# Kernel optimization log

Hardware: AMD Instinct MI355X
Metric: run time of the kernel (lower is better)

Reference implementation:

```python
import jax, jax.numpy as jnp
import numpy as np
from jax.ops import segment_sum

N_NODES = 50000
N_EDGES = 800000
D = 128
N_LAYERS = 3
N_GRAPHS = 256


def setup_inputs() -> dict:
    key = jax.random.key(0)
    k1, k2, k3, k4, k5, k6 = jax.random.split(key, 6)
    feats = jax.random.normal(k1, (N_NODES, D), dtype=jnp.float32)
    src = jax.random.randint(k2, (N_EDGES,), 0, N_NODES)
    dst = jax.random.randint(k3, (N_EDGES,), 0, N_NODES)
    graph_ids = jnp.sort(jax.random.randint(k4, (N_NODES,), 0, N_GRAPHS))
    W = jax.random.normal(k5, (N_LAYERS, D, D), dtype=jnp.float32) / np.float32(np.sqrt(D))
    b = jax.random.normal(k6, (N_LAYERS, D), dtype=jnp.float32) * 0.01
    return {"feats": feats, "W": W, "b": b, "src": src, "dst": dst, "graph_ids": graph_ids}


def reference(feats, W, b, src, dst, graph_ids):
    # DGL GraphConv with norm='both': h' = act(D_in^{-1/2} A D_out^{-1/2} h W + b)
    ones_e = jnp.ones((src.shape[0],), dtype=feats.dtype)
    deg_out = jnp.clip(segment_sum(ones_e, src, num_segments=N_NODES), 1.0)  # [N]
    deg_in = jnp.clip(segment_sum(ones_e, dst, num_segments=N_NODES), 1.0)   # [N]
    norm_out = jax.lax.rsqrt(deg_out)[:, None]  # [N,1]
    norm_in = jax.lax.rsqrt(deg_in)[:, None]    # [N,1]

    h = feats
    for l in range(N_LAYERS):
        hn = h * norm_out                                  # source-side norm
        agg = segment_sum(hn[src], dst, num_segments=N_NODES)  # SpMM gather/scatter
        agg = agg * norm_in                                # dest-side norm
        h = jax.nn.relu(agg @ W[l] + b[l])                 # [N,D]

    # AvgPooling readout: per-graph mean over nodes
    ones_n = jnp.ones((N_NODES,), dtype=h.dtype)
    counts = jnp.clip(segment_sum(ones_n, graph_ids, num_segments=N_GRAPHS), 1.0)
    pooled = segment_sum(h, graph_ids, num_segments=N_GRAPHS) / counts[:, None]
    return pooled  # [N_GRAPHS, D]
```

## Files before the change

### kernel.cpp

```cpp
#include <hip/hip_runtime.h>
#include <hip/hip_fp16.h>

#define DD 128
#define GG 256
#define RANGES 4
#define RSMAX 12544
#define NCHUNK 64

typedef _Float16 half8 __attribute__((ext_vector_type(8)));
typedef float floatx4 __attribute__((ext_vector_type(4)));

__device__ inline uint2 pack_half4(float4 v) {
    __half2 a = __floats2half2_rn(v.x, v.y);
    __half2 b = __floats2half2_rn(v.z, v.w);
    uint2 u;
    u.x = *reinterpret_cast<unsigned int*>(&a);
    u.y = *reinterpret_cast<unsigned int*>(&b);
    return u;
}

__global__ __launch_bounds__(256) void k_key(const int* __restrict__ src, const int* __restrict__ dst,
                                             unsigned int* __restrict__ key, int E) {
    int i = (blockIdx.x * 256 + threadIdx.x) * 4;
    if (i + 3 < E) {
        int4 s4 = *(const int4*)&src[i];
        int4 d4 = *(const int4*)&dst[i];
        uint4 k4;
        k4.x = (unsigned int)s4.x | ((unsigned int)d4.x << 16);
        k4.y = (unsigned int)s4.y | ((unsigned int)d4.y << 16);
        k4.z = (unsigned int)s4.z | ((unsigned int)d4.z << 16);
        k4.w = (unsigned int)s4.w | ((unsigned int)d4.w << 16);
        *(uint4*)&key[i] = k4;
    } else {
        for (int j = 0; j < 4 && i + j < E; ++j)
            key[i + j] = (unsigned int)src[i + j] | ((unsigned int)dst[i + j] << 16);
    }
}

__global__ __launch_bounds__(256) void k_hist2(const unsigned int* __restrict__ key,
                                               unsigned int* __restrict__ pk,
                                               int E, int N, int C, int RS, int L) {
    __shared__ unsigned int h[RSMAX];
    int r = blockIdx.x / C;
    int c = blockIdx.x % C;
    int r0 = r * RS;
    int r1 = min(r0 + RS, N);
    int nb = r1 - r0;
    for (int i = threadIdx.x; i < nb; i += 256) h[i] = 0;
    __syncthreads();
    int e0 = c * L, e1 = min(e0 + L, E);
    for (int e = e0 + threadIdx.x * 4; e < e1; e += 1024) {
        if (e + 3 < e1) {
            uint4 k4 = *(const uint4*)&key[e];
            #pragma unroll
            for (int j = 0; j < 4; ++j) {
                unsigned int kk = (j == 0) ? k4.x : (j == 1) ? k4.y : (j == 2) ? k4.z : k4.w;
                int s = (int)(kk & 0xFFFFu);
                int d = (int)(kk >> 16);
                if (s >= r0 && s < r1) atomicAdd(&h[s - r0], 1u);
                if (d >= r0 && d < r1) atomicAdd(&h[d - r0], 65536u);
            }
        } else {
            for (int j = 0; j < 4 && e + j < e1; ++j) {
                unsigned int kk = key[e + j];
                int s = (int)(kk & 0xFFFFu);
                int d = (int)(kk >> 16);
                if (s >= r0 && s < r1) atomicAdd(&h[s - r0], 1u);
                if (d >= r0 && d < r1) atomicAdd(&h[d - r0], 65536u);
            }
        }
    }
    __syncthreads();
    for (int i = threadIdx.x; i < nb; i += 256)
        pk[(size_t)c * N + r0 + i] = h[i];
}

__global__ __launch_bounds__(256) void k_reduce(const unsigned int* __restrict__ pk,
                                                float* __restrict__ norm_out, float* __restrict__ norm_in,
                                                int* __restrict__ deg_in, int* __restrict__ bsum,
                                                int N, int C) {
    __shared__ int ws[4];
    int n = blockIdx.x * 256 + threadIdx.x;
    int so = 0, si = 0;
    if (n < N) {
        for (int c = 0; c < C; ++c) {
            unsigned int v = pk[(size_t)c * N + n];
            so += (int)(v & 0xFFFFu);
            si += (int)(v >> 16);
        }
        norm_out[n] = rsqrtf(fmaxf((float)so, 1.0f));
        norm_in[n] = rsqrtf(fmaxf((float)si, 1.0f));
        deg_in[n] = si;
    }
    int s = si;
    #pragma unroll
    for (int off = 32; off; off >>= 1) s += __shfl_xor(s, off);
    int lane = threadIdx.x & 63, w = threadIdx.x >> 6;
    if (lane == 0) ws[w] = s;
    __syncthreads();
    if (threadIdx.x == 0) bsum[blockIdx.x] = ws[0] + ws[1] + ws[2] + ws[3];
}

__global__ __launch_bounds__(256) void k_misc(int* bsum, int nblk, int* row_ptr, int N,
                                              const int* __restrict__ gid, int* g_start, int G,
                                              const float* __restrict__ W, __half* __restrict__ Wt,
                                              const float* __restrict__ feats,
                                              const float* __restrict__ norm_out,
                                              uint2* __restrict__ Xh) {
    int blk = blockIdx.x;
    int tid = threadIdx.x;
    if (blk == 0) {
        if (tid < 64) {
            int lane = tid;
            int carry = 0;
            for (int base = 0; base < nblk; base += 64) {
                int i = base + lane;
                int v = (i < nblk) ? bsum[i] : 0;
                int s = v;
                #pragma unroll
                for (int off = 1; off < 64; off <<= 1) {
                    int u = __shfl_up(s, off);
                    if (lane >= off) s += u;
                }
                if (i < nblk) bsum[i] = carry + s - v;
                carry += __shfl(s, 63);
            }
            if (lane == 0) row_ptr[N] = carry;
        }
    } else if (blk <= 2) {
        int g = (blk - 1) * 256 + tid;
        if (g <= G) {
            int lo = 0, hi = N;
            while (lo < hi) {
                int mid = (lo + hi) >> 1;
                if (gid[mid] < g) lo = mid + 1; else hi = mid;
            }
            g_start[g] = lo;
        }
    } else if (blk <= 194) {
        int i = (blk - 3) * 256 + tid;
        if (i < 3 * 16384) {
            int l = i >> 14;
            int rem = i & 16383;
            int n = rem >> 7;
            int k = rem & 127;
            Wt[(size_t)l * 16384 + n * 128 + k] = __float2half(W[(size_t)l * 16384 + k * 128 + n]);
        }
    } else {
        int i = (blk - 195) * 256 + tid;
        if (i < N * 32) {
            int n = i >> 5;
            float4 v = ((const float4*)feats)[i];
            float s = norm_out[n];
            v.x *= s; v.y *= s; v.z *= s; v.w *= s;
            Xh[i] = pack_half4(v);
        }
    }
}

__global__ __launch_bounds__(256) void k_scan_cb(const int* __restrict__ deg, const int* __restrict__ bsum,
                                                 const unsigned int* __restrict__ pk,
                                                 int* __restrict__ row_ptr, int* __restrict__ fbase,
                                                 float* __restrict__ pool0,
                                                 int N, int C) {
    __shared__ int ws[4];
    int t = threadIdx.x;
    if (blockIdx.x < 32) {
        float4 z = make_float4(0.f, 0.f, 0.f, 0.f);
        ((float4*)pool0)[blockIdx.x * 256 + t] = z;
    }
    int n = blockIdx.x * 256 + t;
    int v = (n < N) ? deg[n] : 0;
    int lane = t & 63, w = t >> 6;
    int incl = v;
    #pragma unroll
    for (int off = 1; off < 64; off <<= 1) {
        int u = __shfl_up(incl, off);
        if (lane >= off) incl += u;
    }
    if (lane == 63) ws[w] = incl;
    __syncthreads();
    int woff = 0;
    for (int j = 0; j < w; ++j) woff += ws[j];
    if (n < N) {
        int run = bsum[blockIdx.x] + woff + incl - v;
        row_ptr[n] = run;
        for (int c = 0; c < C; ++c) {
            int h = (int)(pk[(size_t)c * N + n] >> 16);
            fbase[(size_t)c * N + n] = run;
            run += h;
        }
    }
}

__global__ __launch_bounds__(256) void k_fill2(const unsigned int* __restrict__ key,
                                               const int* __restrict__ base, int* __restrict__ col_src,
                                               int E, int N, int C, int RS, int L) {
    __shared__ int cnt[RSMAX];
    int r = blockIdx.x / C;
    int c = blockIdx.x % C;
    int r0 = r * RS;
    int r1 = min(r0 + RS, N);
    int nb = r1 - r0;
    const int* bc = base + (size_t)c * N;
    for (int i = threadIdx.x; i < nb; i += 256) cnt[i] = bc[r0 + i];
    __syncthreads();
    int e0 = c * L, e1 = min(e0 + L, E);
    for (int e = e0 + threadIdx.x * 4; e < e1; e += 1024) {
        if (e + 3 < e1) {
            uint4 k4 = *(const uint4*)&key[e];
            #pragma unroll
            for (int j = 0; j < 4; ++j) {
                unsigned int kk = (j == 0) ? k4.x : (j == 1) ? k4.y : (j == 2) ? k4.z : k4.w;
                int s = (int)(kk & 0xFFFFu);
                int d = (int)(kk >> 16);
                if (d >= r0 && d < r1) { int o = atomicAdd(&cnt[d - r0], 1); col_src[o] = s; }
            }
        } else {
            for (int j = 0; j < 4 && e + j < e1; ++j) {
                unsigned int kk = key[e + j];
                int s = (int)(kk & 0xFFFFu);
                int d = (int)(kk >> 16);
                if (d >= r0 && d < r1) { int o = atomicAdd(&cnt[d - r0], 1); col_src[o] = s; }
            }
        }
    }
}

__device__ inline void acc_row(float* acc, uint4 u) {
    const __half2* h = (const __half2*)&u;
    #pragma unroll
    for (int i = 0; i < 4; ++i) {
        float2 f = __half22float2(h[i]);
        acc[2 * i] += f.x;
        acc[2 * i + 1] += f.y;
    }
}

__global__ __launch_bounds__(256, 8) void k_agg_mm(
    const uint4* __restrict__ Xin, const float* __restrict__ norm_in,
    const int* __restrict__ row_ptr, const int* __restrict__ col_src,
    const __half* __restrict__ Wt, const float* __restrict__ bl,
    const float* __restrict__ scale, __half* __restrict__ Xout,
    float* __restrict__ pool_out, const int* __restrict__ gid,
    const int* __restrict__ g_start, int N) {
    __shared__ _Float16 Ah[16 * 136];
    int t = threadIdx.x;
    int n0 = blockIdx.x * 16;
    int l16 = t & 15;
    int grp = t >> 4;
    int n = n0 + grp;

    float acc[8] = {};
    if (n < N) {
        int beg = row_ptr[n], end = row_ptr[n + 1];
        int k = beg;
        bool have = (k + 3 < end);
        int4 s = make_int4(0, 0, 0, 0);
        if (have) s = *(const int4*)&col_src[k];
        while (have) {
            int kn = k + 4;
            bool haven = (kn + 3 < end);
            int4 sn = s;
            if (haven) sn = *(const int4*)&col_src[kn];
            uint4 u0 = Xin[(size_t)s.x * 16 + l16];
            uint4 u1 = Xin[(size_t)s.y * 16 + l16];
            uint4 u2 = Xin[(size_t)s.z * 16 + l16];
            uint4 u3 = Xin[(size_t)s.w * 16 + l16];
            acc_row(acc, u0);
            acc_row(acc, u1);
            acc_row(acc, u2);
            acc_row(acc, u3);
            s = sn; k = kn; have = haven;
        }
        for (; k < end; ++k) {
            uint4 u = Xin[(size_t)col_src[k] * 16 + l16];
            acc_row(acc, u);
        }
        float ni = norm_in[n];
        #pragma unroll
        for (int i = 0; i < 8; ++i) acc[i] *= ni;
    }
    __half2 hp[4];
    #pragma unroll
    for (int i = 0; i < 4; ++i) hp[i] = __floats2half2_rn(acc[2 * i], acc[2 * i + 1]);
    *(uint4*)&Ah[grp * 136 + l16 * 8] = *(const uint4*)hp;
    __syncthreads();

    int wave = t >> 6;
    int lane = t & 63;
    int quad = lane >> 4;
    int mrow = lane & 15;

    half8 af[4];
    #pragma unroll
    for (int kc = 0; kc < 4; ++kc)
        af[kc] = *(const half8*)&Ah[mrow * 136 + kc * 32 + quad * 8];

    floatx4 Cc[2];
    Cc[0] = (floatx4){0.f, 0.f, 0.f, 0.f};
    Cc[1] = (floatx4){0.f, 0.f, 0.f, 0.f};
    #pragma unroll
    for (int ct = 0; ct < 2; ++ct) {
        int col = wave * 32 + ct * 16 + mrow;
        #pragma unroll
        for (int kc = 0; kc < 4; ++kc) {
            half8 bf = *(const half8*)&Wt[(size_t)col * 128 + kc * 32 + quad * 8];
            Cc[ct] = __builtin_amdgcn_mfma_f32_16x16x32_f16(af[kc], bf, Cc[ct], 0, 0, 0);
        }
    }

    if (Xout) {
        float sc[4];
        #pragma unroll
        for (int r = 0; r < 4; ++r) {
            int node = n0 + quad * 4 + r;
            sc[r] = (node < N) ? scale[node] : 1.0f;
        }
        #pragma unroll
        for (int ct = 0; ct < 2; ++ct) {
            int col = wave * 32 + ct * 16 + mrow;
            float bias = bl[col];
            #pragma unroll
            for (int r = 0; r < 4; ++r) {
                int node = n0 + quad * 4 + r;
                if (node < N)
                    Xout[(size_t)node * 128 + col] =
                        __float2half(fmaxf(Cc[ct][r] + bias, 0.f) * sc[r]);
            }
        }
    } else {
        int nlast = min(n0 + 15, N - 1);
        int ga = (n0 < N) ? gid[n0] : -1;
        int gb = (n0 < N) ? gid[nlast] : -2;
        if (ga == gb && ga >= 0) {
            float inv = 1.f / fmaxf((float)(g_start[ga + 1] - g_start[ga]), 1.f);
            #pragma unroll
            for (int ct = 0; ct < 2; ++ct) {
                int col = wave * 32 + ct * 16 + mrow;
                float bias = bl[col];
                float s = 0.f;
                #pragma unroll
                for (int r = 0; r < 4; ++r) {
                    int node = n0 + quad * 4 + r;
                    if (node < N) s += fmaxf(Cc[ct][r] + bias, 0.f);
                }
                s += __shfl_xor(s, 16);
                s += __shfl_xor(s, 32);
                if (quad == 0) atomicAdd(&pool_out[(size_t)ga * DD + col], s * inv);
            }
        } else {
            int garr[4];
            #pragma unroll
            for (int r = 0; r < 4; ++r) {
                int node = n0 + quad * 4 + r;
                garr[r] = (node < N) ? gid[node] : -1;
            }
            #pragma unroll
            for (int ct = 0; ct < 2; ++ct) {
                int col = wave * 32 + ct * 16 + mrow;
                float bias = bl[col];
                float s = 0.f;
                int gcur = -1;
                #pragma unroll
                for (int r = 0; r < 4; ++r) {
                    if (garr[r] >= 0) {
                        float val = fmaxf(Cc[ct][r] + bias, 0.f);
                        if (garr[r] != gcur) {
                            if (gcur >= 0) {
                                float cnt = fmaxf((float)(g_start[gcur + 1] - g_start[gcur]), 1.f);
                                atomicAdd(&pool_out[(size_t)gcur * DD + col], s / cnt);
                            }
                            gcur = garr[r];
                            s = 0.f;
                        }
                        s += val;
                    }
                }
                if (gcur >= 0) {
                    float cnt = fmaxf((float)(g_start[gcur + 1] - g_start[gcur]), 1.f);
                    atomicAdd(&pool_out[(size_t)gcur * DD + col], s / cnt);
                }
            }
        }
    }
}

extern "C" void kernel_launch(void* const* d_in, const int* in_sizes, int n_in,
                              void* d_out, int out_size, void* d_ws, size_t ws_size,
                              hipStream_t stream) {
    const float* feats = (const float*)d_in[0];
    const float* W = (const float*)d_in[1];
    const float* b = (const float*)d_in[2];
    const int* src = (const int*)d_in[3];
    const int* dst = (const int*)d_in[4];
    const int* gid = (const int*)d_in[5];
    float* out = (float*)d_out;
    const int N = in_sizes[0] / DD;
    const int E = in_sizes[3];

    const int C = NCHUNK;
    const int RS = (N + RANGES - 1) / RANGES;
    const int L = (((E + C - 1) / C) + 3) & ~3;

    char* ws = (char*)d_ws;
    size_t off = 0;
    auto take = [&](size_t bytes) {
        char* p = ws + off;
        off = (off + bytes + 255) & ~(size_t)255;
        return p;
    };
    float* norm_out = (float*)take((size_t)N * 4);
    float* norm_in  = (float*)take((size_t)N * 4);
    int*   deg_in   = (int*)take((size_t)N * 4);
    int*   row_ptr  = (int*)take((size_t)(N + 1) * 4);
    int*   col_src  = (int*)take((size_t)E * 4);
    int*   g_start  = (int*)take((size_t)(GG + 1) * 4);
    int*   bsum     = (int*)take((size_t)1024 * 4);
    unsigned int* key = (unsigned int*)take((size_t)E * 4);
    __half* Wth     = (__half*)take((size_t)3 * 16384 * 2);
    uint4* Xh       = (uint4*)take((size_t)N * DD * 2);
    uint4* Yh       = (uint4*)take((size_t)N * DD * 2);
    size_t chunk_arr = ((size_t)C * N * 4 + 255) & ~(size_t)255;
    char* uni = take(2 * chunk_arr);
    unsigned int* pk = (unsigned int*)uni;
    int* fbase = (int*)(uni + chunk_arr);

    const int nblk = (N + 255) / 256;
    const int mgrid_misc = 195 + (N * 32 + 255) / 256;

    k_key<<<(E + 1023) / 1024, 256, 0, stream>>>(src, dst, key, E);
    k_hist2<<<RANGES * C, 256, 0, stream>>>(key, pk, E, N, C, RS, L);
    k_reduce<<<nblk, 256, 0, stream>>>(pk, norm_out, norm_in, deg_in, bsum, N, C);
    k_misc<<<mgrid_misc, 256, 0, stream>>>(bsum, nblk, row_ptr, N, gid, g_start, GG,
                                           W, Wth, feats, norm_out, (uint2*)Xh);
    k_scan_cb<<<nblk, 256, 0, stream>>>(deg_in, bsum, pk, row_ptr, fbase, out, N, C);
    k_fill2<<<RANGES * C, 256, 0, stream>>>(key, fbase, col_src, E, N, C, RS, L);

    const int agrid = (N + 15) / 16;
    for (int l = 0; l < 3; ++l) {
        const __half* Wtl = Wth + (size_t)l * 16384;
        const float* blp = b + (size_t)l * DD;
        const uint4* Xi = (l == 1) ? Yh : Xh;
        if (l < 2) {
            __half* Xo = (__half*)((l == 0) ? Yh : Xh);
            k_agg_mm<<<agrid, 256, 0, stream>>>(Xi, norm_in, row_ptr, col_src, Wtl, blp,
                                                norm_out, Xo, nullptr, nullptr, nullptr, N);
        } else {
            k_agg_mm<<<agrid, 256, 0, stream>>>(Xi, norm_in, row_ptr, col_src, Wtl, blp,
                                                nullptr, nullptr, out, gid, g_start, N);
        }
    }
}
```

Measured before the change: 264.2 us.

## Permute nodes by graph and in-degree bucket for balanced aggregation blocks

Builds a node permutation by counting-sorting nodes on a (graph id, clamped in-degree) key, using a histogram, a prefix scan in the misc kernel, and atomic placement in the scan kernel. The aggregate-matmul kernel then processes nodes in permuted order, so each 16-node block holds nodes of similar degree within the same graph, which is meant to reduce load imbalance between the per-node groups. Rows are written back to their original node index. This adds histogram atomics, an indirection load per node, and scattered output writes, and the atomic placement makes node order within a bin nondeterministic.

```diff
diff --git a/kernel.cpp b/kernel.cpp
--- a/kernel.cpp
+++ b/kernel.cpp
@@ -6,6 +6,7 @@
 #define RANGES 4
 #define RSMAX 12544
 #define NCHUNK 64
+#define DBINS 16384
 
 typedef _Float16 half8 __attribute__((ext_vector_type(8)));
 typedef float floatx4 __attribute__((ext_vector_type(4)));
@@ -20,8 +21,10 @@
 }
 
 __global__ __launch_bounds__(256) void k_key(const int* __restrict__ src, const int* __restrict__ dst,
-                                             unsigned int* __restrict__ key, int E) {
-    int i = (blockIdx.x * 256 + threadIdx.x) * 4;
+                                             unsigned int* __restrict__ key, int* __restrict__ dbin, int E) {
+    int z = blockIdx.x * 256 + threadIdx.x;
+    if (z < DBINS / 4) ((int4*)dbin)[z] = make_int4(0, 0, 0, 0);
+    int i = z * 4;
     if (i + 3 < E) {
         int4 s4 = *(const int4*)&src[i];
         int4 d4 = *(const int4*)&dst[i];
@@ -76,8 +79,10 @@
 }
 
 __global__ __launch_bounds__(256) void k_reduce(const unsigned int* __restrict__ pk,
+                                                const int* __restrict__ gid,
                                                 float* __restrict__ norm_out, float* __restrict__ norm_in,
                                                 int* __restrict__ deg_in, int* __restrict__ bsum,
+                                                int* __restrict__ dbin,
                                                 int N, int C) {
     __shared__ int ws[4];
     int n = blockIdx.x * 256 + threadIdx.x;
@@ -91,6 +96,8 @@
         norm_out[n] = rsqrtf(fmaxf((float)so, 1.0f));
         norm_in[n] = rsqrtf(fmaxf((float)si, 1.0f));
         deg_in[n] = si;
+        int key = (gid[n] << 6) | min(si, 63);
+        atomicAdd(&dbin[key], 1);
     }
     int s = si;
     #pragma unroll
@@ -106,6 +113,7 @@
                                               const float* __restrict__ W, __half* __restrict__ Wt,
                                               const float* __restrict__ feats,
                                               const float* __restrict__ norm_out,
+                                              int* __restrict__ dbin,
                                               uint2* __restrict__ Xh) {
     int blk = blockIdx.x;
     int tid = threadIdx.x;
@@ -127,6 +135,27 @@
             }
             if (lane == 0) row_ptr[N] = carry;
         }
+        __shared__ int wsum[4];
+        int base2 = tid * 64;
+        int s2 = 0;
+        for (int j = 0; j < 64; ++j) s2 += dbin[base2 + j];
+        int lane = tid & 63, wv = tid >> 6;
+        int incl = s2;
+        #pragma unroll
+        for (int off = 1; off < 64; off <<= 1) {
+            int u = __shfl_up(incl, off);
+            if (lane >= off) incl += u;
+        }
+        if (lane == 63) wsum[wv] = incl;
+        __syncthreads();
+        int woff = 0;
+        for (int j = 0; j < wv; ++j) woff += wsum[j];
+        int run = woff + incl - s2;
+        for (int j = 0; j < 64; ++j) {
+            int v = dbin[base2 + j];
+            dbin[base2 + j] = run;
+            run += v;
+        }
     } else if (blk <= 2) {
         int g = (blk - 1) * 256 + tid;
         if (g <= G) {
@@ -160,7 +189,9 @@
 
 __global__ __launch_bounds__(256) void k_scan_cb(const int* __restrict__ deg, const int* __restrict__ bsum,
                                                  const unsigned int* __restrict__ pk,
+                                                 const int* __restrict__ gid,
                                                  int* __restrict__ row_ptr, int* __restrict__ fbase,
+                                                 int* __restrict__ dbin, int* __restrict__ perm,
                                                  float* __restrict__ pool0,
                                                  int N, int C) {
     __shared__ int ws[4];
@@ -190,6 +221,9 @@
             fbase[(size_t)c * N + n] = run;
             run += h;
         }
+        int key = (gid[n] << 6) | min(v, 63);
+        int pos = atomicAdd(&dbin[key], 1);
+        perm[pos] = n;
     }
 }
 
@@ -240,6 +274,7 @@
 __global__ __launch_bounds__(256, 8) void k_agg_mm(
     const uint4* __restrict__ Xin, const float* __restrict__ norm_in,
     const int* __restrict__ row_ptr, const int* __restrict__ col_src,
+    const int* __restrict__ perm,
     const __half* __restrict__ Wt, const float* __restrict__ bl,
     const float* __restrict__ scale, __half* __restrict__ Xout,
     float* __restrict__ pool_out, const int* __restrict__ gid,
@@ -249,7 +284,8 @@
     int n0 = blockIdx.x * 16;
     int l16 = t & 15;
     int grp = t >> 4;
-    int n = n0 + grp;
+    int pn = n0 + grp;
+    int n = (pn < N) ? perm[pn] : N;
 
     float acc[8] = {};
     if (n < N) {
@@ -311,11 +347,13 @@
     }
 
     if (Xout) {
+        int nd[4];
         float sc[4];
         #pragma unroll
         for (int r = 0; r < 4; ++r) {
-            int node = n0 + quad * 4 + r;
-            sc[r] = (node < N) ? scale[node] : 1.0f;
+            int pr = n0 + quad * 4 + r;
+            nd[r] = (pr < N) ? perm[pr] : N;
+            sc[r] = (nd[r] < N) ? scale[nd[r]] : 1.0f;
         }
         #pragma unroll
         for (int ct = 0; ct < 2; ++ct) {
@@ -323,16 +361,15 @@
             float bias = bl[col];
             #pragma unroll
             for (int r = 0; r < 4; ++r) {
-                int node = n0 + quad * 4 + r;
-                if (node < N)
-                    Xout[(size_t)node * 128 + col] =
+                if (nd[r] < N)
+                    Xout[(size_t)nd[r] * 128 + col] =
                         __float2half(fmaxf(Cc[ct][r] + bias, 0.f) * sc[r]);
             }
         }
     } else {
         int nlast = min(n0 + 15, N - 1);
-        int ga = (n0 < N) ? gid[n0] : -1;
-        int gb = (n0 < N) ? gid[nlast] : -2;
+        int ga = (n0 < N) ? gid[perm[n0]] : -1;
+        int gb = (n0 < N) ? gid[perm[nlast]] : -2;
         if (ga == gb && ga >= 0) {
             float inv = 1.f / fmaxf((float)(g_start[ga + 1] - g_start[ga]), 1.f);
             #pragma unroll
@@ -342,8 +379,8 @@
                 float s = 0.f;
                 #pragma unroll
                 for (int r = 0; r < 4; ++r) {
-                    int node = n0 + quad * 4 + r;
-                    if (node < N) s += fmaxf(Cc[ct][r] + bias, 0.f);
+                    int pr = n0 + quad * 4 + r;
+                    if (pr < N) s += fmaxf(Cc[ct][r] + bias, 0.f);
                 }
                 s += __shfl_xor(s, 16);
                 s += __shfl_xor(s, 32);
@@ -353,8 +390,8 @@
             int garr[4];
             #pragma unroll
             for (int r = 0; r < 4; ++r) {
-                int node = n0 + quad * 4 + r;
-                garr[r] = (node < N) ? gid[node] : -1;
+                int pr = n0 + quad * 4 + r;
+                garr[r] = (pr < N) ? gid[perm[pr]] : -1;
             }
             #pragma unroll
             for (int ct = 0; ct < 2; ++ct) {
@@ -417,6 +454,8 @@
     int*   col_src  = (int*)take((size_t)E * 4);
     int*   g_start  = (int*)take((size_t)(GG + 1) * 4);
     int*   bsum     = (int*)take((size_t)1024 * 4);
+    int*   dbin     = (int*)take((size_t)DBINS * 4);
+    int*   perm     = (int*)take((size_t)N * 4);
     unsigned int* key = (unsigned int*)take((size_t)E * 4);
     __half* Wth     = (__half*)take((size_t)3 * 16384 * 2);
     uint4* Xh       = (uint4*)take((size_t)N * DD * 2);
@@ -429,12 +468,13 @@
     const int nblk = (N + 255) / 256;
     const int mgrid_misc = 195 + (N * 32 + 255) / 256;
 
-    k_key<<<(E + 1023) / 1024, 256, 0, stream>>>(src, dst, key, E);
+    k_key<<<(E + 1023) / 1024, 256, 0, stream>>>(src, dst, key, dbin, E);
     k_hist2<<<RANGES * C, 256, 0, stream>>>(key, pk, E, N, C, RS, L);
-    k_reduce<<<nblk, 256, 0, stream>>>(pk, norm_out, norm_in, deg_in, bsum, N, C);
+    k_reduce<<<nblk, 256, 0, stream>>>(pk, gid, norm_out, norm_in, deg_in, bsum, dbin, N, C);
     k_misc<<<mgrid_misc, 256, 0, stream>>>(bsum, nblk, row_ptr, N, gid, g_start, GG,
-                                           W, Wth, feats, norm_out, (uint2*)Xh);
-    k_scan_cb<<<nblk, 256, 0, stream>>>(deg_in, bsum, pk, row_ptr, fbase, out, N, C);
+                                           W, Wth, feats, norm_out, dbin, (uint2*)Xh);
+    k_scan_cb<<<nblk, 256, 0, stream>>>(deg_in, bsum, pk, gid, row_ptr, fbase, dbin, perm,
+                                        out, N, C);
     k_fill2<<<RANGES * C, 256, 0, stream>>>(key, fbase, col_src, E, N, C, RS, L);
 
     const int agrid = (N + 15) / 16;
@@ -444,10 +484,10 @@
         const uint4* Xi = (l == 1) ? Yh : Xh;
         if (l < 2) {
             __half* Xo = (__half*)((l == 0) ? Yh : Xh);
-            k_agg_mm<<<agrid, 256, 0, stream>>>(Xi, norm_in, row_ptr, col_src, Wtl, blp,
+            k_agg_mm<<<agrid, 256, 0, stream>>>(Xi, norm_in, row_ptr, col_src, perm, Wtl, blp,
                                                 norm_out, Xo, nullptr, nullptr, nullptr, N);
         } else {
-            k_agg_mm<<<agrid, 256, 0, stream>>>(Xi, norm_in, row_ptr, col_src, Wtl, blp,
+            k_agg_mm<<<agrid, 256, 0, stream>>>(Xi, norm_in, row_ptr, col_src, perm, Wtl, blp,
                                                 nullptr, nullptr, out, gid, g_start, N);
         }
     }
```

Measured after the change: 278.1 us. 1.05x slower.

## Replace chunked LDS histogram and fill with global-atomic degree count and CSR fill

Applied to the files above, without the earlier changes.

The CSR build drops the per-chunk shared-memory histograms and the per-chunk base offsets. Degrees are now counted directly with global atomics while the packed keys are built, and the fill step uses one global cursor per destination node with atomicAdd. This removes the C×N partial arrays, their reduction and scan loops, and two kernels' worth of redundant key passes. In exchange it adds a zeroing kernel and relies on contended global atomics. The order of entries within a row is now nondeterministic, which can slightly change floating-point summation order.

```diff
diff --git a/kernel.cpp b/kernel.cpp
--- a/kernel.cpp
+++ b/kernel.cpp
@@ -3,9 +3,6 @@
 
 #define DD 128
 #define GG 256
-#define RANGES 4
-#define RSMAX 12544
-#define NCHUNK 64
 
 typedef _Float16 half8 __attribute__((ext_vector_type(8)));
 typedef float floatx4 __attribute__((ext_vector_type(4)));
@@ -19,8 +16,19 @@
     return u;
 }
 
-__global__ __launch_bounds__(256) void k_key(const int* __restrict__ src, const int* __restrict__ dst,
-                                             unsigned int* __restrict__ key, int E) {
+__global__ __launch_bounds__(256) void k_zero(uint4* __restrict__ pk4, float4* __restrict__ out4,
+                                              int npk4, int nout4) {
+    int i = blockIdx.x * 256 + threadIdx.x;
+    if (i < npk4) pk4[i] = make_uint4(0, 0, 0, 0);
+    else {
+        int j = i - npk4;
+        if (j < nout4) out4[j] = make_float4(0.f, 0.f, 0.f, 0.f);
+    }
+}
+
+__global__ __launch_bounds__(256) void k_key_hist(const int* __restrict__ src, const int* __restrict__ dst,
+                                                  unsigned int* __restrict__ key,
+                                                  unsigned int* __restrict__ pk, int E) {
     int i = (blockIdx.x * 256 + threadIdx.x) * 4;
     if (i + 3 < E) {
         int4 s4 = *(const int4*)&src[i];
@@ -31,63 +39,34 @@
         k4.z = (unsigned int)s4.z | ((unsigned int)d4.z << 16);
         k4.w = (unsigned int)s4.w | ((unsigned int)d4.w << 16);
         *(uint4*)&key[i] = k4;
+        atomicAdd(&pk[s4.x], 1u);
+        atomicAdd(&pk[s4.y], 1u);
+        atomicAdd(&pk[s4.z], 1u);
+        atomicAdd(&pk[s4.w], 1u);
+        atomicAdd(&pk[d4.x], 65536u);
+        atomicAdd(&pk[d4.y], 65536u);
+        atomicAdd(&pk[d4.z], 65536u);
+        atomicAdd(&pk[d4.w], 65536u);
     } else {
-        for (int j = 0; j < 4 && i + j < E; ++j)
-            key[i + j] = (unsigned int)src[i + j] | ((unsigned int)dst[i + j] << 16);
-    }
-}
-
-__global__ __launch_bounds__(256) void k_hist2(const unsigned int* __restrict__ key,
-                                               unsigned int* __restrict__ pk,
-                                               int E, int N, int C, int RS, int L) {
-    __shared__ unsigned int h[RSMAX];
-    int r = blockIdx.x / C;
-    int c = blockIdx.x % C;
-    int r0 = r * RS;
-    int r1 = min(r0 + RS, N);
-    int nb = r1 - r0;
-    for (int i = threadIdx.x; i < nb; i += 256) h[i] = 0;
-    __syncthreads();
-    int e0 = c * L, e1 = min(e0 + L, E);
-    for (int e = e0 + threadIdx.x * 4; e < e1; e += 1024) {
-        if (e + 3 < e1) {
-            uint4 k4 = *(const uint4*)&key[e];
-            #pragma unroll
-            for (int j = 0; j < 4; ++j) {
-                unsigned int kk = (j == 0) ? k4.x : (j == 1) ? k4.y : (j == 2) ? k4.z : k4.w;
-                int s = (int)(kk & 0xFFFFu);
-                int d = (int)(kk >> 16);
-                if (s >= r0 && s < r1) atomicAdd(&h[s - r0], 1u);
-                if (d >= r0 && d < r1) atomicAdd(&h[d - r0], 65536u);
-            }
-        } else {
-            for (int j = 0; j < 4 && e + j < e1; ++j) {
-                unsigned int kk = key[e + j];
-                int s = (int)(kk & 0xFFFFu);
-                int d = (int)(kk >> 16);
-                if (s >= r0 && s < r1) atomicAdd(&h[s - r0], 1u);
-                if (d >= r0 && d < r1) atomicAdd(&h[d - r0], 65536u);
-            }
-        }
-    }
-    __syncthreads();
-    for (int i = threadIdx.x; i < nb; i += 256)
-        pk[(size_t)c * N + r0 + i] = h[i];
-}
-
-__global__ __launch_bounds__(256) void k_reduce(const unsigned int* __restrict__ pk,
-                                                float* __restrict__ norm_out, float* __restrict__ norm_in,
-                                                int* __restrict__ deg_in, int* __restrict__ bsum,
-                                                int N, int C) {
+        for (int j = 0; j < 4 && i + j < E; ++j) {
+            int s = src[i + j], d = dst[i + j];
+            key[i + j] = (unsigned int)s | ((unsigned int)d << 16);
+            atomicAdd(&pk[s], 1u);
+            atomicAdd(&pk[d], 65536u);
+        }
+    }
+}
+
+__global__ __launch_bounds__(256) void k_scanA(const unsigned int* __restrict__ pk,
+                                               float* __restrict__ norm_out, float* __restrict__ norm_in,
+                                               int* __restrict__ deg_in, int* __restrict__ bsum, int N) {
     __shared__ int ws[4];
     int n = blockIdx.x * 256 + threadIdx.x;
-    int so = 0, si = 0;
+    int si = 0;
     if (n < N) {
-        for (int c = 0; c < C; ++c) {
-            unsigned int v = pk[(size_t)c * N + n];
-            so += (int)(v & 0xFFFFu);
-            si += (int)(v >> 16);
-        }
+        unsigned int v = pk[n];
+        int so = (int)(v & 0xFFFFu);
+        si = (int)(v >> 16);
         norm_out[n] = rsqrtf(fmaxf((float)so, 1.0f));
         norm_in[n] = rsqrtf(fmaxf((float)si, 1.0f));
         deg_in[n] = si;
@@ -158,17 +137,10 @@
     }
 }
 
-__global__ __launch_bounds__(256) void k_scan_cb(const int* __restrict__ deg, const int* __restrict__ bsum,
-                                                 const unsigned int* __restrict__ pk,
-                                                 int* __restrict__ row_ptr, int* __restrict__ fbase,
-                                                 float* __restrict__ pool0,
-                                                 int N, int C) {
+__global__ __launch_bounds__(256) void k_scanB(const int* __restrict__ deg, const int* __restrict__ bsum,
+                                               int* __restrict__ row_ptr, int* __restrict__ cursor, int N) {
     __shared__ int ws[4];
     int t = threadIdx.x;
-    if (blockIdx.x < 32) {
-        float4 z = make_float4(0.f, 0.f, 0.f, 0.f);
-        ((float4*)pool0)[blockIdx.x * 256 + t] = z;
-    }
     int n = blockIdx.x * 256 + t;
     int v = (n < N) ? deg[n] : 0;
     int lane = t & 63, w = t >> 6;
@@ -185,44 +157,30 @@
     if (n < N) {
         int run = bsum[blockIdx.x] + woff + incl - v;
         row_ptr[n] = run;
-        for (int c = 0; c < C; ++c) {
-            int h = (int)(pk[(size_t)c * N + n] >> 16);
-            fbase[(size_t)c * N + n] = run;
-            run += h;
-        }
-    }
-}
-
-__global__ __launch_bounds__(256) void k_fill2(const unsigned int* __restrict__ key,
-                                               const int* __restrict__ base, int* __restrict__ col_src,
-                                               int E, int N, int C, int RS, int L) {
-    __shared__ int cnt[RSMAX];
-    int r = blockIdx.x / C;
-    int c = blockIdx.x % C;
-    int r0 = r * RS;
-    int r1 = min(r0 + RS, N);
-    int nb = r1 - r0;
-    const int* bc = base + (size_t)c * N;
-    for (int i = threadIdx.x; i < nb; i += 256) cnt[i] = bc[r0 + i];
-    __syncthreads();
-    int e0 = c * L, e1 = min(e0 + L, E);
-    for (int e = e0 + threadIdx.x * 4; e < e1; e += 1024) {
-        if (e + 3 < e1) {
-            uint4 k4 = *(const uint4*)&key[e];
-            #pragma unroll
-            for (int j = 0; j < 4; ++j) {
-                unsigned int kk = (j == 0) ? k4.x : (j == 1) ? k4.y : (j == 2) ? k4.z : k4.w;
-                int s = (int)(kk & 0xFFFFu);
-                int d = (int)(kk >> 16);
-                if (d >= r0 && d < r1) { int o = atomicAdd(&cnt[d - r0], 1); col_src[o] = s; }
-            }
-        } else {
-            for (int j = 0; j < 4 && e + j < e1; ++j) {
-                unsigned int kk = key[e + j];
-                int s = (int)(kk & 0xFFFFu);
-                int d = (int)(kk >> 16);
-                if (d >= r0 && d < r1) { int o = atomicAdd(&cnt[d - r0], 1); col_src[o] = s; }
-            }
+        cursor[n] = run;
+    }
+}
+
+__global__ __launch_bounds__(256) void k_fill(const unsigned int* __restrict__ key,
+                                              int* __restrict__ cursor, int* __restrict__ col_src, int E) {
+    int i = (blockIdx.x * 256 + threadIdx.x) * 4;
+    if (i + 3 < E) {
+        uint4 k4 = *(const uint4*)&key[i];
+        #pragma unroll
+        for (int j = 0; j < 4; ++j) {
+            unsigned int kk = (j == 0) ? k4.x : (j == 1) ? k4.y : (j == 2) ? k4.z : k4.w;
+            int s = (int)(kk & 0xFFFFu);
+            int d = (int)(kk >> 16);
+            int o = atomicAdd(&cursor[d], 1);
+            col_src[o] = s;
+        }
+    } else {
+        for (int j = 0; j < 4 && i + j < E; ++j) {
+            unsigned int kk = key[i + j];
+            int s = (int)(kk & 0xFFFFu);
+            int d = (int)(kk >> 16);
+            int o = atomicAdd(&cursor[d], 1);
+            col_src[o] = s;
         }
     }
 }
@@ -399,10 +357,6 @@
     const int N = in_sizes[0] / DD;
     const int E = in_sizes[3];
 
-    const int C = NCHUNK;
-    const int RS = (N + RANGES - 1) / RANGES;
-    const int L = (((E + C - 1) / C) + 3) & ~3;
-
     char* ws = (char*)d_ws;
     size_t off = 0;
     auto take = [&](size_t bytes) {
@@ -414,28 +368,29 @@
     float* norm_in  = (float*)take((size_t)N * 4);
     int*   deg_in   = (int*)take((size_t)N * 4);
     int*   row_ptr  = (int*)take((size_t)(N + 1) * 4);
+    int*   cursor   = (int*)take((size_t)N * 4);
     int*   col_src  = (int*)take((size_t)E * 4);
     int*   g_start  = (int*)take((size_t)(GG + 1) * 4);
     int*   bsum     = (int*)take((size_t)1024 * 4);
+    unsigned int* pk = (unsigned int*)take((size_t)N * 4);
     unsigned int* key = (unsigned int*)take((size_t)E * 4);
     __half* Wth     = (__half*)take((size_t)3 * 16384 * 2);
     uint4* Xh       = (uint4*)take((size_t)N * DD * 2);
     uint4* Yh       = (uint4*)take((size_t)N * DD * 2);
-    size_t chunk_arr = ((size_t)C * N * 4 + 255) & ~(size_t)255;
-    char* uni = take(2 * chunk_arr);
-    unsigned int* pk = (unsigned int*)uni;
-    int* fbase = (int*)(uni + chunk_arr);
 
     const int nblk = (N + 255) / 256;
     const int mgrid_misc = 195 + (N * 32 + 255) / 256;
-
-    k_key<<<(E + 1023) / 1024, 256, 0, stream>>>(src, dst, key, E);
-    k_hist2<<<RANGES * C, 256, 0, stream>>>(key, pk, E, N, C, RS, L);
-    k_reduce<<<nblk, 256, 0, stream>>>(pk, norm_out, norm_in, deg_in, bsum, N, C);
+    const int npk4 = (N + 3) / 4;
+    const int nout4 = GG * DD / 4;
+    const int zgrid = (npk4 + nout4 + 255) / 256;
+
+    k_zero<<<zgrid, 256, 0, stream>>>((uint4*)pk, (float4*)out, npk4, nout4);
+    k_key_hist<<<(E + 1023) / 1024, 256, 0, stream>>>(src, dst, key, pk, E);
+    k_scanA<<<nblk, 256, 0, stream>>>(pk, norm_out, norm_in, deg_in, bsum, N);
     k_misc<<<mgrid_misc, 256, 0, stream>>>(bsum, nblk, row_ptr, N, gid, g_start, GG,
                                            W, Wth, feats, norm_out, (uint2*)Xh);
-    k_scan_cb<<<nblk, 256, 0, stream>>>(deg_in, bsum, pk, row_ptr, fbase, out, N, C);
-    k_fill2<<<RANGES * C, 256, 0, stream>>>(key, fbase, col_src, E, N, C, RS, L);
+    k_scanB<<<nblk, 256, 0, stream>>>(deg_in, bsum, row_ptr, cursor, N);
+    k_fill<<<(E + 1023) / 1024, 256, 0, stream>>>(key, cursor, col_src, E);
 
     const int agrid = (N + 15) / 16;
     for (int l = 0; l < 3; ++l) {
```

After: 327.7 us. +24.0%, slower.
